# Performance work log

Hardware: AMD Instinct MI355X
Metric: run time of the kernel (lower is better)

The kernel has to match this reference:

```python
import jax, jax.numpy as jnp
import numpy as np

N = 50000
E = 800000
F_IN = 256
HID = 64
HEADS = 4
CLASSES = 8
NEG_SLOPE = 0.2  # PyG GATConv default


def setup_inputs() -> dict:
    key = jax.random.key(0)
    ks = jax.random.split(key, 10)
    x = jax.random.normal(ks[0], (N, F_IN), jnp.float32)
    edge_index = jax.random.randint(ks[1], (2, E), 0, N, dtype=jnp.int32)
    # layer 1: feature -> hidden, heads=4, concat
    W1 = jax.random.normal(ks[2], (F_IN, HEADS * HID), jnp.float32) / np.sqrt(F_IN).astype(np.float32)
    att1_src = jax.random.normal(ks[3], (HEADS, HID), jnp.float32) / np.sqrt(HID).astype(np.float32)
    att1_dst = jax.random.normal(ks[4], (HEADS, HID), jnp.float32) / np.sqrt(HID).astype(np.float32)
    b1 = jnp.zeros((HEADS * HID,), jnp.float32)
    # layer 2: hidden*heads -> classes, heads=1
    W2 = jax.random.normal(ks[5], (HEADS * HID, CLASSES), jnp.float32) / np.sqrt(HEADS * HID).astype(np.float32)
    att2_src = jax.random.normal(ks[6], (1, CLASSES), jnp.float32) / np.sqrt(CLASSES).astype(np.float32)
    att2_dst = jax.random.normal(ks[7], (1, CLASSES), jnp.float32) / np.sqrt(CLASSES).astype(np.float32)
    b2 = jnp.zeros((CLASSES,), jnp.float32)
    return {"x": x, "edge_index": edge_index, "W1": W1, "att1_src": att1_src,
            "att1_dst": att1_dst, "b1": b1, "W2": W2, "att2_src": att2_src,
            "att2_dst": att2_dst, "b2": b2}


def _gat_conv(x, W, a_src, a_dst, b, src, dst, heads, ch, n):
    # h: [N, H, C] per-head projected features
    h = (x @ W).reshape(n, heads, ch)
    alpha_src = jnp.einsum('nhc,hc->nh', h, a_src)  # [N, H]
    alpha_dst = jnp.einsum('nhc,hc->nh', h, a_dst)  # [N, H]
    # per-edge attention logits (gather along edges)
    e = jax.nn.leaky_relu(alpha_src[src] + alpha_dst[dst], NEG_SLOPE)  # [E, H]
    # segment softmax over edges sharing a destination node
    e_max = jax.ops.segment_max(e, dst, num_segments=n)  # [N, H]
    ex = jnp.exp(e - e_max[dst])
    denom = jax.ops.segment_sum(ex, dst, num_segments=n)  # [N, H]
    alpha = ex / denom[dst]  # self-loops guarantee denom > 0
    # weighted scatter-sum of source messages
    out = jax.ops.segment_sum(alpha[..., None] * h[src], dst, num_segments=n)  # [N, H, C]
    return out.reshape(n, heads * ch) + b


def reference(x, edge_index, W1, att1_src, att1_dst, b1, W2, att2_src, att2_dst, b2):
    n = x.shape[0]
    # PyG GATConv adds self-loops by default
    loop = jnp.arange(n, dtype=edge_index.dtype)
    src = jnp.concatenate([edge_index[0], loop])
    dst = jnp.concatenate([edge_index[1], loop])
    h = _gat_conv(x, W1, att1_src, att1_dst, b1, src, dst, HEADS, HID, n)
    h = jax.nn.relu(h)
    # dropout is identity in eval mode (training=self.training)
    out = _gat_conv(h, W2, att2_src, att2_dst, b2, src, dst, 1, CLASSES, n)
    return jax.nn.log_softmax(out, axis=1)
```

## Files before the change

### kernel.cpp

```cpp
#include <hip/hip_runtime.h>
#include <math.h>

#define NNODES 50000
#define NEDGES 800000
#define ETOT   850000
#define SLOPE  0.2f
#define BSLOTS 96
#define CPAD   16
#define NTILE  782
#define BBLK   518

typedef unsigned short ushort_t;
typedef unsigned int   uint_t;
typedef unsigned char  uchar_t;
typedef __attribute__((ext_vector_type(8))) __bf16 bf16x8;
typedef __attribute__((ext_vector_type(4))) float  floatx4;
typedef __attribute__((ext_vector_type(2))) float  floatx2;

#if defined(__has_builtin)
#if __has_builtin(__builtin_amdgcn_cvt_pk_f32_fp8) && __has_builtin(__builtin_amdgcn_cvt_pk_fp8_f32)
#define HWFP8 1
#endif
#endif

__device__ __forceinline__ float leaky(float v) { return fmaxf(v, SLOPE * v); }

__device__ __forceinline__ ushort_t f2bf(float f) {
    uint_t u = __float_as_uint(f);
    uint_t r = (u + 0x7fffu + ((u >> 16) & 1u)) >> 16;
    return (ushort_t)r;
}

__device__ __forceinline__ uint_t f2fp8_sw(float f) {
    uint_t u = __float_as_uint(f);
    uint_t s = (u >> 24) & 0x80u;
    u &= 0x7fffffffu;
    u = u + 0x7ffffu + ((u >> 20) & 1u);
    int e8 = (int)(u >> 23) - 120;
    uint_t m3 = (u >> 20) & 7u;
    if (e8 <= 0) return s;
    if (e8 >= 16) return s | 0x7eu;
    return s | ((uint_t)e8 << 3) | m3;
}
__device__ __forceinline__ float fp8tof_sw(uint_t b) {
    uint_t t = (b & 0x7fu) << 4;
    uint_t r = ((b & 0x80u) << 8) | (t + 0x3C00u);
    return (t >= 0x80u) ? __uint_as_float(r << 16) : 0.f;
}

__device__ __forceinline__ uint_t pk4fp8(float a, float b, float c, float d) {
#ifdef HWFP8
    int pk = 0;
    pk = __builtin_amdgcn_cvt_pk_fp8_f32(a, b, pk, false);
    pk = __builtin_amdgcn_cvt_pk_fp8_f32(c, d, pk, true);
    return (uint_t)pk;
#else
    return f2fp8_sw(a) | (f2fp8_sw(b) << 8) | (f2fp8_sw(c) << 16) | (f2fp8_sw(d) << 24);
#endif
}

__device__ __forceinline__ void dec8acc(uint2 v, float w, float* acc) {
#ifdef HWFP8
    floatx2 f0 = __builtin_amdgcn_cvt_pk_f32_fp8((int)v.x, false);
    floatx2 f1 = __builtin_amdgcn_cvt_pk_f32_fp8((int)v.x, true);
    floatx2 f2 = __builtin_amdgcn_cvt_pk_f32_fp8((int)v.y, false);
    floatx2 f3 = __builtin_amdgcn_cvt_pk_f32_fp8((int)v.y, true);
    acc[0] += w * f0.x; acc[1] += w * f0.y;
    acc[2] += w * f1.x; acc[3] += w * f1.y;
    acc[4] += w * f2.x; acc[5] += w * f2.y;
    acc[6] += w * f3.x; acc[7] += w * f3.y;
#else
    acc[0] += w * fp8tof_sw(v.x & 0xffu);
    acc[1] += w * fp8tof_sw((v.x >> 8) & 0xffu);
    acc[2] += w * fp8tof_sw((v.x >> 16) & 0xffu);
    acc[3] += w * fp8tof_sw(v.x >> 24);
    acc[4] += w * fp8tof_sw(v.y & 0xffu);
    acc[5] += w * fp8tof_sw((v.y >> 8) & 0xffu);
    acc[6] += w * fp8tof_sw((v.y >> 16) & 0xffu);
    acc[7] += w * fp8tof_sw(v.y >> 24);
#endif
}

__device__ __forceinline__ float hsel(float4 v, int h) {
    float t0 = (h & 1) ? v.y : v.x;
    float t1 = (h & 1) ? v.w : v.z;
    return (h & 2) ? t1 : t0;
}

__device__ __forceinline__ int esrc(const int* ei, int e) { return e < NEDGES ? ei[e]          : e - NEDGES; }
__device__ __forceinline__ int edst(const int* ei, int e) { return e < NEDGES ? ei[NEDGES + e] : e - NEDGES; }

__global__ void prep_k(const float* __restrict__ W1, ushort_t* __restrict__ W1c,
                       const float* __restrict__ b1, const float* __restrict__ W2,
                       float* __restrict__ b1p, float* __restrict__ W2p,
                       int* __restrict__ cnt) {
    int bid = blockIdx.x, tid = threadIdx.x;
    int gtid = bid * 256 + tid;
    if (bid < 256) {
        int k = gtid >> 8, n = gtid & 255;
        W1c[(k >> 5) * 8192 + n * 32 + (k & 31)] = f2bf(W1[gtid]);
    } else if (bid == 256) {
        int chp = tid;
        int q = chp & 63, cc = q >> 2, t = q & 3;
        int ch = (chp & 192) | (t * 16 + cc);
        b1p[chp] = b1[ch];
        #pragma unroll
        for (int j = 0; j < 8; ++j) W2p[chp * 8 + j] = W2[ch * 8 + j];
    }
    for (int i = gtid; i < NNODES * CPAD; i += 257 * 256) cnt[i] = 0;
}

__global__ __launch_bounds__(256) void gb_k(const float* __restrict__ X,
                                            const ushort_t* __restrict__ W1c,
                                            const float* __restrict__ att_s,
                                            const float* __restrict__ att_d,
                                            uchar_t* __restrict__ h1f,
                                            float* __restrict__ as1,
                                            float* __restrict__ ad1,
                                            const int* __restrict__ ei,
                                            int* __restrict__ cnt,
                                            int* __restrict__ bkt) {
    __shared__ ushort_t Als[64 * 40];
    int tid = threadIdx.x;

    if (blockIdx.x >= NTILE) {
        for (int e = (blockIdx.x - NTILE) * 256 + tid; e < ETOT; e += BBLK * 256) {
            int d = edst(ei, e), s = esrc(ei, e);
            int pos = atomicAdd(&cnt[d * CPAD], 1);
            if (pos < BSLOTS) bkt[d * BSLOTS + pos] = s;
        }
        return;
    }

    int row0 = blockIdx.x * 64;
    int wv = tid >> 6, lane = tid & 63, c15 = lane & 15, quad = lane >> 4;
    floatx4 acc[4][4] = {};

    int r = tid >> 3, c4 = tid & 7;
    int rowA = row0 + r, rowB = row0 + r + 32;
    float4 pa0 = make_float4(0.f, 0.f, 0.f, 0.f);
    float4 pa1 = make_float4(0.f, 0.f, 0.f, 0.f);
    if (rowA < NNODES) pa0 = *(const float4*)&X[(size_t)rowA * 256 + c4 * 4];
    if (rowB < NNODES) pa1 = *(const float4*)&X[(size_t)rowB * 256 + c4 * 4];

    for (int kc = 0; kc < 8; ++kc) {
        if (kc) __syncthreads();
        {
            uint2 pk;
            pk.x = (uint_t)f2bf(pa0.x) | ((uint_t)f2bf(pa0.y) << 16);
            pk.y = (uint_t)f2bf(pa0.z) | ((uint_t)f2bf(pa0.w) << 16);
            *(uint2*)&Als[r * 40 + c4 * 4] = pk;
            pk.x = (uint_t)f2bf(pa1.x) | ((uint_t)f2bf(pa1.y) << 16);
            pk.y = (uint_t)f2bf(pa1.z) | ((uint_t)f2bf(pa1.w) << 16);
            *(uint2*)&Als[(r + 32) * 40 + c4 * 4] = pk;
        }
        __syncthreads();
        if (kc < 7) {
            pa0 = make_float4(0.f, 0.f, 0.f, 0.f);
            pa1 = make_float4(0.f, 0.f, 0.f, 0.f);
            if (rowA < NNODES) pa0 = *(const float4*)&X[(size_t)rowA * 256 + (kc + 1) * 32 + c4 * 4];
            if (rowB < NNODES) pa1 = *(const float4*)&X[(size_t)rowB * 256 + (kc + 1) * 32 + c4 * 4];
        }
        uint4 af[4], bfr[4];
        #pragma unroll
        for (int t = 0; t < 4; ++t)
            af[t] = *(const uint4*)&Als[(t * 16 + c15) * 40 + quad * 8];
        #pragma unroll
        for (int t = 0; t < 4; ++t)
            bfr[t] = *(const uint4*)&W1c[kc * 8192 + (wv * 64 + t * 16 + c15) * 32 + quad * 8];
        #pragma unroll
        for (int tm = 0; tm < 4; ++tm)
            #pragma unroll
            for (int tn = 0; tn < 4; ++tn)
                acc[tm][tn] = __builtin_amdgcn_mfma_f32_16x16x32_bf16(
                    __builtin_bit_cast(bf16x8, af[tm]),
                    __builtin_bit_cast(bf16x8, bfr[tn]),
                    acc[tm][tn], 0, 0, 0);
    }

    float asv[4], adv[4];
    #pragma unroll
    for (int tn = 0; tn < 4; ++tn) {
        asv[tn] = att_s[wv * 64 + tn * 16 + c15];
        adv[tn] = att_d[wv * 64 + tn * 16 + c15];
    }
    float ps[4][4], pd[4][4];
    #pragma unroll
    for (int tm = 0; tm < 4; ++tm)
        #pragma unroll
        for (int r2 = 0; r2 < 4; ++r2) {
            float vs = 0.f, vd = 0.f;
            #pragma unroll
            for (int tn = 0; tn < 4; ++tn) {
                float a = acc[tm][tn][r2];
                vs += a * asv[tn]; vd += a * adv[tn];
            }
            ps[tm][r2] = vs; pd[tm][r2] = vd;
        }
    #pragma unroll
    for (int tm = 0; tm < 4; ++tm) {
        #pragma unroll
        for (int r2 = 0; r2 < 4; ++r2) {
            int row = row0 + tm * 16 + quad * 4 + r2;
            if (row < NNODES) {
                uint_t pk = pk4fp8(acc[tm][0][r2], acc[tm][1][r2],
                                   acc[tm][2][r2], acc[tm][3][r2]);
                *(uint_t*)&h1f[(size_t)row * 256 + wv * 64 + c15 * 4] = pk;
            }
        }
    }
    #pragma unroll
    for (int off = 1; off < 16; off <<= 1)
        #pragma unroll
        for (int tm = 0; tm < 4; ++tm)
            #pragma unroll
            for (int r2 = 0; r2 < 4; ++r2) {
                ps[tm][r2] += __shfl_xor(ps[tm][r2], off, 64);
                pd[tm][r2] += __shfl_xor(pd[tm][r2], off, 64);
            }
    if (c15 == 0) {
        #pragma unroll
        for (int tm = 0; tm < 4; ++tm)
            #pragma unroll
            for (int r2 = 0; r2 < 4; ++r2) {
                int row = row0 + tm * 16 + quad * 4 + r2;
                if (row < NNODES) {
                    as1[row * 4 + wv] = ps[tm][r2];
                    ad1[row * 4 + wv] = pd[tm][r2];
                }
            }
    }
}

#define PREL(BASE, VV)                                                          \
    {                                                                           \
        _Pragma("unroll")                                                       \
        for (int u = 0; u < 8; ++u) {                                           \
            int e = (BASE) + u;                                                 \
            int se = __shfl(s_reg, sbase + e, 64);                              \
            if (e < deg)                                                        \
                VV[u] = *(const uint2*)&h1f[(size_t)se * 256 + l32 * 8];        \
        }                                                                       \
    }
#define PREW(BASE, WW)                                                          \
    {                                                                           \
        _Pragma("unroll")                                                       \
        for (int u = 0; u < 8; ++u) WW[u] = wls[wv][half][(BASE) + u][h];       \
    }
#define CONS(BASE, VV, WW)                                                      \
    {                                                                           \
        _Pragma("unroll")                                                       \
        for (int u = 0; u < 8; ++u) {                                           \
            if ((BASE) + u < deg) dec8acc(VV[u], WW[u], acc);                   \
        }                                                                       \
    }

__global__ __launch_bounds__(256) void f1_k(const int* __restrict__ cnt,
                                            const int* __restrict__ bkt,
                                            const float* __restrict__ as1,
                                            const float* __restrict__ ad1,
                                            const uchar_t* __restrict__ h1f,
                                            const float* __restrict__ b1p,
                                            const float* __restrict__ W2p,
                                            const float* __restrict__ a2sw,
                                            const float* __restrict__ a2dw,
                                            float* __restrict__ h2,
                                            float* __restrict__ a2s,
                                            float* __restrict__ a2d) {
    int wv = threadIdx.x >> 6;
    int lane = threadIdx.x & 63;
    int half = lane >> 5, l32 = lane & 31;
    int node = blockIdx.x * 8 + wv * 2 + half;
    int h = l32 >> 3;
    int deg = min(cnt[node * CPAD], BSLOTS);
    const int* bp = bkt + (size_t)node * BSLOTS;
    float4 advec = *(const float4*)&ad1[(size_t)node * 4];
    __shared__ float wls[4][2][32][4];

    float acc[8] = {};
    float dn0, dn1, dn2, dn3;
    if (deg <= 32) {
        bool act = l32 < deg;
        int s_reg = node;
        if (act) s_reg = bp[l32];
        int sbase = half << 5;
        uint2 va[8], vb[8];
        float wa[8], wb[8];

        float4 av = *(const float4*)&as1[(size_t)s_reg * 4];
        PREL(0, va);
        if (deg > 8) PREL(8, vb);

        float e0 = act ? __expf(leaky(av.x + advec.x)) : 0.f;
        float e1 = act ? __expf(leaky(av.y + advec.y)) : 0.f;
        float e2 = act ? __expf(leaky(av.z + advec.z)) : 0.f;
        float e3 = act ? __expf(leaky(av.w + advec.w)) : 0.f;
        *(float4*)&wls[wv][half][l32][0] = make_float4(e0, e1, e2, e3);
        dn0 = e0; dn1 = e1; dn2 = e2; dn3 = e3;
        #pragma unroll
        for (int off = 16; off; off >>= 1) {
            dn0 += __shfl_xor(dn0, off, 64);
            dn1 += __shfl_xor(dn1, off, 64);
            dn2 += __shfl_xor(dn2, off, 64);
            dn3 += __shfl_xor(dn3, off, 64);
        }
        PREW(0, wa);
        if (deg > 8) PREW(8, wb);

        CONS(0, va, wa);
        if (deg > 8) {
            if (deg > 16) { PREL(16, va); PREW(16, wa); }
            CONS(8, vb, wb);
            if (deg > 16) {
                if (deg > 24) { PREL(24, vb); PREW(24, wb); }
                CONS(16, va, wa);
                if (deg > 24) CONS(24, vb, wb);
            }
        }
    } else {
        dn0 = dn1 = dn2 = dn3 = 0.f;
        for (int j = l32; j < deg; j += 32) {
            int s = bp[j];
            float4 av = *(const float4*)&as1[(size_t)s * 4];
            dn0 += __expf(leaky(av.x + advec.x));
            dn1 += __expf(leaky(av.y + advec.y));
            dn2 += __expf(leaky(av.z + advec.z));
            dn3 += __expf(leaky(av.w + advec.w));
        }
        #pragma unroll
        for (int off = 16; off; off >>= 1) {
            dn0 += __shfl_xor(dn0, off, 64);
            dn1 += __shfl_xor(dn1, off, 64);
            dn2 += __shfl_xor(dn2, off, 64);
            dn3 += __shfl_xor(dn3, off, 64);
        }
        float advh = hsel(advec, h);
        int cmax = deg - 1;
        for (int base = 0; base < deg; base += 8) {
            #pragma unroll
            for (int u = 0; u < 8; ++u) {
                int e = base + u;
                int ce = min(e, cmax);
                int se = bp[ce];
                float ash = as1[(size_t)se * 4 + h];
                float w = (e < deg) ? __expf(leaky(ash + advh)) : 0.f;
                uint2 v = *(const uint2*)&h1f[(size_t)se * 256 + l32 * 8];
                dec8acc(v, w, acc);
            }
        }
    }
    float rdh = 1.f / hsel(make_float4(dn0, dn1, dn2, dn3), h);
    #pragma unroll
    for (int c = 0; c < 8; ++c) acc[c] *= rdh;

    int k0 = l32 * 8;
    float4 ba = *(const float4*)&b1p[k0];
    float4 bb = *(const float4*)&b1p[k0 + 4];
    float xv[8];
    xv[0] = fmaxf(acc[0] + ba.x, 0.f); xv[1] = fmaxf(acc[1] + ba.y, 0.f);
    xv[2] = fmaxf(acc[2] + ba.z, 0.f); xv[3] = fmaxf(acc[3] + ba.w, 0.f);
    xv[4] = fmaxf(acc[4] + bb.x, 0.f); xv[5] = fmaxf(acc[5] + bb.y, 0.f);
    xv[6] = fmaxf(acc[6] + bb.z, 0.f); xv[7] = fmaxf(acc[7] + bb.w, 0.f);
    float p[8] = {};
    #pragma unroll
    for (int q = 0; q < 8; ++q) {
        const float4* w2p = (const float4*)&W2p[(size_t)(k0 + q) * 8];
        float4 wa2 = w2p[0], wb2 = w2p[1];
        p[0] += xv[q] * wa2.x; p[1] += xv[q] * wa2.y; p[2] += xv[q] * wa2.z; p[3] += xv[q] * wa2.w;
        p[4] += xv[q] * wb2.x; p[5] += xv[q] * wb2.y; p[6] += xv[q] * wb2.z; p[7] += xv[q] * wb2.w;
    }
    #pragma unroll
    for (int off = 16; off; off >>= 1)
        #pragma unroll
        for (int c = 0; c < 8; ++c) p[c] += __shfl_xor(p[c], off, 64);
    if (l32 == 0) {
        *(float4*)&h2[(size_t)node * 8]     = make_float4(p[0], p[1], p[2], p[3]);
        *(float4*)&h2[(size_t)node * 8 + 4] = make_float4(p[4], p[5], p[6], p[7]);
        float vs = 0.f, vd = 0.f;
        #pragma unroll
        for (int c = 0; c < 8; ++c) { vs += p[c] * a2sw[c]; vd += p[c] * a2dw[c]; }
        a2s[node] = vs; a2d[node] = vd;
    }
}

__global__ __launch_bounds__(256) void f2_k(const int* __restrict__ cnt,
                                            const int* __restrict__ bkt,
                                            const float* __restrict__ a2s,
                                            const float* __restrict__ a2d,
                                            const float* __restrict__ h2,
                                            const float* __restrict__ b2,
                                            float* __restrict__ out) {
    int wv = threadIdx.x >> 6;
    int lane = threadIdx.x & 63;
    int half = lane >> 5, l32 = lane & 31;
    int node = blockIdx.x * 8 + wv * 2 + half;
    int deg = min(cnt[node * CPAD], BSLOTS);
    const int* bp = bkt + (size_t)node * BSLOTS;
    float adv = a2d[node];

    float acc_a = 0.f, acc_b = 0.f;
    float den;
    int c = l32 & 7, eg = l32 >> 3;
    if (deg <= 32) {
        bool act = l32 < deg;
        int s_reg = node;
        if (act) s_reg = bp[l32];
        float ex = act ? __expf(leaky(a2s[s_reg] + adv)) : 0.f;
        den = ex;
        #pragma unroll
        for (int off = 16; off; off >>= 1) den += __shfl_xor(den, off, 64);
        int nb = (deg + 7) & ~7;
        int sbase = half << 5;
        for (int base = 0; base < nb; base += 8) {
            int e1 = base + eg, e2 = base + 4 + eg;
            int se1 = __shfl(s_reg, sbase + e1, 64);
            float w1 = __shfl(ex,    sbase + e1, 64);
            int se2 = __shfl(s_reg, sbase + e2, 64);
            float w2 = __shfl(ex,    sbase + e2, 64);
            acc_a += w1 * h2[(size_t)se1 * 8 + c];
            acc_b += w2 * h2[(size_t)se2 * 8 + c];
        }
    } else {
        den = 0.f;
        for (int j = l32; j < deg; j += 32) {
            int s = bp[j];
            den += __expf(leaky(a2s[s] + adv));
        }
        #pragma unroll
        for (int off = 16; off; off >>= 1) den += __shfl_xor(den, off, 64);
        int cmax = deg - 1;
        for (int base = 0; base < deg; base += 4) {
            int e = base + eg, ce = min(e, cmax);
            int se = bp[ce];
            float w = (e < deg) ? __expf(leaky(a2s[se] + adv)) : 0.f;
            acc_a += w * h2[(size_t)se * 8 + c];
        }
    }
    float acc = acc_a + acc_b;
    acc += __shfl_xor(acc, 8, 64);
    acc += __shfl_xor(acc, 16, 64);
    acc /= den;

    float v = acc + b2[c];
    float mx = v;
    #pragma unroll
    for (int off = 1; off < 8; off <<= 1) mx = fmaxf(mx, __shfl_xor(mx, off, 64));
    float ex2 = __expf(v - mx);
    float ss = ex2;
    #pragma unroll
    for (int off = 1; off < 8; off <<= 1) ss += __shfl_xor(ss, off, 64);
    if (l32 < 8) out[(size_t)node * 8 + c] = v - (mx + __logf(ss));
}

extern "C" void kernel_launch(void* const* d_in, const int* in_sizes, int n_in,
                              void* d_out, int out_size, void* d_ws, size_t ws_size,
                              hipStream_t stream) {
    const float* x    = (const float*)d_in[0];
    const int*   ei   = (const int*)  d_in[1];
    const float* W1   = (const float*)d_in[2];
    const float* a1sw = (const float*)d_in[3];
    const float* a1dw = (const float*)d_in[4];
    const float* b1   = (const float*)d_in[5];
    const float* W2   = (const float*)d_in[6];
    const float* a2sw = (const float*)d_in[7];
    const float* a2dw = (const float*)d_in[8];
    const float* b2   = (const float*)d_in[9];
    float* out = (float*)d_out;

    uchar_t* h1f = (uchar_t*)d_ws;
    ushort_t* W1c = (ushort_t*)(h1f + 12800000);
    float* as1  = (float*)(W1c + 65536);
    float* ad1  = as1 + 200000;
    float* h2   = ad1 + 200000;
    float* a2s  = h2  + 400000;
    float* a2d  = a2s + 50000;
    float* b1p  = a2d + 50000;
    float* W2p  = b1p + 256;
    int*   cnt  = (int*)(W2p + 2048);
    int*   bkt  = cnt + NNODES * CPAD;

    prep_k<<<257, 256, 0, stream>>>(W1, W1c, b1, W2, b1p, W2p, cnt);

    gb_k<<<NTILE + BBLK, 256, 0, stream>>>(x, W1c, a1sw, a1dw, h1f, as1, ad1,
                                           ei, cnt, bkt);

    f1_k<<<NNODES / 8, 256, 0, stream>>>(cnt, bkt, as1, ad1, h1f, b1p, W2p,
                                         a2sw, a2dw, h2, a2s, a2d);

    f2_k<<<NNODES / 8, 256, 0, stream>>>(cnt, bkt, a2s, a2d, h2, b2, out);
}
```

Before: 254.1 us.

## Replicate per-node edge counters into four sub-buckets to reduce atomic contention

Bucketing now spreads each destination's atomic counter across four replicas selected by edge index, each owning a 24-slot segment of the node's bucket, and the bucketing loop is unrolled by two. The consumer kernels read four counters and map a logical neighbour index to its segment slot. The zeroing loop is widened to int4 stores over the larger counter array. This aims to reduce same-address atomic serialisation, at the cost of extra counter reads, slot arithmetic per neighbour lookup, and a lower per-segment cap that can drop edges for high-degree nodes.

```diff
diff --git a/kernel.cpp b/kernel.cpp
--- a/kernel.cpp
+++ b/kernel.cpp
@@ -6,6 +6,8 @@
 #define ETOT   850000
 #define SLOPE  0.2f
 #define BSLOTS 96
+#define SEGCAP 24
+#define NREP   4
 #define CPAD   16
 #define NTILE  782
 #define BBLK   518
@@ -90,6 +92,12 @@
 __device__ __forceinline__ int esrc(const int* ei, int e) { return e < NEDGES ? ei[e]          : e - NEDGES; }
 __device__ __forceinline__ int edst(const int* ei, int e) { return e < NEDGES ? ei[NEDGES + e] : e - NEDGES; }
 
+__device__ __forceinline__ int slot_of(int j, int p1, int p2, int p3) {
+    int seg = (j >= p1) + (j >= p2) + (j >= p3);
+    int base = seg == 0 ? 0 : (seg == 1 ? p1 : (seg == 2 ? p2 : p3));
+    return seg * SEGCAP + (j - base);
+}
+
 __global__ void prep_k(const float* __restrict__ W1, ushort_t* __restrict__ W1c,
                        const float* __restrict__ b1, const float* __restrict__ W2,
                        float* __restrict__ b1p, float* __restrict__ W2p,
@@ -107,7 +115,9 @@
         #pragma unroll
         for (int j = 0; j < 8; ++j) W2p[chp * 8 + j] = W2[ch * 8 + j];
     }
-    for (int i = gtid; i < NNODES * CPAD; i += 257 * 256) cnt[i] = 0;
+    int4* cz = (int4*)cnt;
+    int4 z = make_int4(0, 0, 0, 0);
+    for (int i = gtid; i < NNODES * CPAD; i += 257 * 256) cz[i] = z;
 }
 
 __global__ __launch_bounds__(256) void gb_k(const float* __restrict__ X,
@@ -124,10 +134,23 @@
     int tid = threadIdx.x;
 
     if (blockIdx.x >= NTILE) {
-        for (int e = (blockIdx.x - NTILE) * 256 + tid; e < ETOT; e += BBLK * 256) {
+        const int stride = BBLK * 256;
+        int e = (blockIdx.x - NTILE) * 256 + tid;
+        for (; e + stride < ETOT; e += 2 * stride) {
+            int e2 = e + stride;
+            int d1 = edst(ei, e),  s1 = esrc(ei, e);
+            int d2 = edst(ei, e2), s2 = esrc(ei, e2);
+            int r1 = e & 3, r2 = e2 & 3;
+            int p1 = atomicAdd(&cnt[((size_t)r1 * NNODES + d1) * CPAD], 1);
+            int p2 = atomicAdd(&cnt[((size_t)r2 * NNODES + d2) * CPAD], 1);
+            if (p1 < SEGCAP) bkt[d1 * BSLOTS + r1 * SEGCAP + p1] = s1;
+            if (p2 < SEGCAP) bkt[d2 * BSLOTS + r2 * SEGCAP + p2] = s2;
+        }
+        for (; e < ETOT; e += stride) {
             int d = edst(ei, e), s = esrc(ei, e);
-            int pos = atomicAdd(&cnt[d * CPAD], 1);
-            if (pos < BSLOTS) bkt[d * BSLOTS + pos] = s;
+            int r = e & 3;
+            int pos = atomicAdd(&cnt[((size_t)r * NNODES + d) * CPAD], 1);
+            if (pos < SEGCAP) bkt[d * BSLOTS + r * SEGCAP + pos] = s;
         }
         return;
     }
@@ -272,9 +295,15 @@
     int half = lane >> 5, l32 = lane & 31;
     int node = blockIdx.x * 8 + wv * 2 + half;
     int h = l32 >> 3;
-    int deg = min(cnt[node * CPAD], BSLOTS);
-    const int* bp = bkt + (size_t)node * BSLOTS;
+
+    int c0 = cnt[(size_t)node * CPAD];
+    int c1 = cnt[((size_t)NNODES + node) * CPAD];
+    int c2 = cnt[((size_t)2 * NNODES + node) * CPAD];
+    int c3 = cnt[((size_t)3 * NNODES + node) * CPAD];
     float4 advec = *(const float4*)&ad1[(size_t)node * 4];
+    c0 = min(c0, SEGCAP); c1 = min(c1, SEGCAP); c2 = min(c2, SEGCAP); c3 = min(c3, SEGCAP);
+    int p1 = c0, p2 = c0 + c1, p3 = p2 + c2;
+    int deg = p3 + c3;
     __shared__ float wls[4][2][32][4];
 
     float acc[8] = {};
@@ -282,7 +311,7 @@
     if (deg <= 32) {
         bool act = l32 < deg;
         int s_reg = node;
-        if (act) s_reg = bp[l32];
+        if (act) s_reg = bkt[(size_t)node * BSLOTS + slot_of(l32, p1, p2, p3)];
         int sbase = half << 5;
         uint2 va[8], vb[8];
         float wa[8], wb[8];
@@ -320,7 +349,7 @@
     } else {
         dn0 = dn1 = dn2 = dn3 = 0.f;
         for (int j = l32; j < deg; j += 32) {
-            int s = bp[j];
+            int s = bkt[(size_t)node * BSLOTS + slot_of(j, p1, p2, p3)];
             float4 av = *(const float4*)&as1[(size_t)s * 4];
             dn0 += __expf(leaky(av.x + advec.x));
             dn1 += __expf(leaky(av.y + advec.y));
@@ -341,7 +370,7 @@
             for (int u = 0; u < 8; ++u) {
                 int e = base + u;
                 int ce = min(e, cmax);
-                int se = bp[ce];
+                int se = bkt[(size_t)node * BSLOTS + slot_of(ce, p1, p2, p3)];
                 float ash = as1[(size_t)se * 4 + h];
                 float w = (e < deg) ? __expf(leaky(ash + advh)) : 0.f;
                 uint2 v = *(const uint2*)&h1f[(size_t)se * 256 + l32 * 8];
@@ -394,9 +423,15 @@
     int lane = threadIdx.x & 63;
     int half = lane >> 5, l32 = lane & 31;
     int node = blockIdx.x * 8 + wv * 2 + half;
-    int deg = min(cnt[node * CPAD], BSLOTS);
-    const int* bp = bkt + (size_t)node * BSLOTS;
+
+    int c0 = cnt[(size_t)node * CPAD];
+    int c1 = cnt[((size_t)NNODES + node) * CPAD];
+    int c2 = cnt[((size_t)2 * NNODES + node) * CPAD];
+    int c3 = cnt[((size_t)3 * NNODES + node) * CPAD];
     float adv = a2d[node];
+    c0 = min(c0, SEGCAP); c1 = min(c1, SEGCAP); c2 = min(c2, SEGCAP); c3 = min(c3, SEGCAP);
+    int p1 = c0, p2 = c0 + c1, p3 = p2 + c2;
+    int deg = p3 + c3;
 
     float acc_a = 0.f, acc_b = 0.f;
     float den;
@@ -404,7 +439,7 @@
     if (deg <= 32) {
         bool act = l32 < deg;
         int s_reg = node;
-        if (act) s_reg = bp[l32];
+        if (act) s_reg = bkt[(size_t)node * BSLOTS + slot_of(l32, p1, p2, p3)];
         float ex = act ? __expf(leaky(a2s[s_reg] + adv)) : 0.f;
         den = ex;
         #pragma unroll
@@ -423,7 +458,7 @@
     } else {
         den = 0.f;
         for (int j = l32; j < deg; j += 32) {
-            int s = bp[j];
+            int s = bkt[(size_t)node * BSLOTS + slot_of(j, p1, p2, p3)];
             den += __expf(leaky(a2s[s] + adv));
         }
         #pragma unroll
@@ -431,7 +466,7 @@
         int cmax = deg - 1;
         for (int base = 0; base < deg; base += 4) {
             int e = base + eg, ce = min(e, cmax);
-            int se = bp[ce];
+            int se = bkt[(size_t)node * BSLOTS + slot_of(ce, p1, p2, p3)];
             float w = (e < deg) ? __expf(leaky(a2s[se] + adv)) : 0.f;
             acc_a += w * h2[(size_t)se * 8 + c];
         }
@@ -477,7 +512,7 @@
     float* b1p  = a2d + 50000;
     float* W2p  = b1p + 256;
     int*   cnt  = (int*)(W2p + 2048);
-    int*   bkt  = cnt + NNODES * CPAD;
+    int*   bkt  = cnt + (size_t)NREP * NNODES * CPAD;
 
     prep_k<<<257, 256, 0, stream>>>(W1, W1c, b1, W2, b1p, W2p, cnt);
 
```

Measured after the change: 257.9 us. About the same (+1.5%).
